# Performance work log

Hardware: AMD Instinct MI355X
Metric: run time of the kernel (lower is better)

## Reference

```python
import jax, jax.numpy as jnp
import numpy as np

L, B, D, V = 4096, 4, 512, 1000  # seq_len, batch, hidden_dim, index_dim


def setup_inputs() -> dict:
    key = jax.random.key(0)
    k0, k1, k2, k3, k4 = jax.random.split(key, 5)
    s_d = 1.0 / np.sqrt(D)
    return {
        "x": jax.random.normal(k0, (L, B, D), dtype=jnp.float32),
        # ctc_weight: nn.Linear(D, D)
        "Ww": jax.random.uniform(k1, (D, D), dtype=jnp.float32, minval=-s_d, maxval=s_d),
        "Wb": jax.random.uniform(k2, (D,), dtype=jnp.float32, minval=-s_d, maxval=s_d),
        # ctc_linear: nn.Linear(D, V)
        "Lw": jax.random.uniform(k3, (V, D), dtype=jnp.float32, minval=-s_d, maxval=s_d),
        "Lb": jax.random.uniform(k4, (V,), dtype=jnp.float32, minval=-s_d, maxval=s_d),
    }


def reference(x, Ww, Wb, Lw, Lb):
    # x: (L, B, D) -> (B, L, D)
    xb = jnp.transpose(x, (1, 0, 2))
    # ctc_weight(x): (B, L, D)
    wx = xb @ Ww.T + Wb
    # bmm(x, W(x)^T): (B, L, L) bilinear scores (no softmax)
    scores = jnp.einsum('bld,bmd->blm', xb, wx)
    # bmm(scores, x): (B, L, D)
    y = jnp.einsum('blm,bmd->bld', scores, xb)
    # ctc_linear + log_softmax over vocab
    logits = y @ Lw.T + Lb  # (B, L, V)
    out = jax.nn.log_softmax(logits, axis=2)
    # permute back to (L, B, V)
    return jnp.transpose(out, (1, 0, 2))
```

## Files before the change

kernel.cpp:

```cpp
#include <hip/hip_runtime.h>
#include <math.h>

#define L_ 4096
#define B_ 4
#define D_ 512
#define V_ 1000
#define VP 1024
#define BD 2048
#define NCH 8

typedef __attribute__((ext_vector_type(8))) short short8;
typedef __attribute__((ext_vector_type(4))) float f32x4;
typedef __attribute__((ext_vector_type(4))) short short4v;

__device__ __forceinline__ short f2bf(float f) {
  unsigned u = __float_as_uint(f);
  unsigned r = (u + 0x7FFFu + ((u >> 16) & 1u)) >> 16;
  return (short)r;
}
__device__ __forceinline__ float bf2f(short v) {
  return __uint_as_float(((unsigned)(unsigned short)v) << 16);
}

__global__ __launch_bounds__(256) void kPre(const float* __restrict__ x,
                                            const float* __restrict__ Wb,
                                            short* __restrict__ xbf,
                                            short* __restrict__ xT,
                                            float* __restrict__ s,
                                            float* __restrict__ c) {
  const int l0 = blockIdx.x * 64, d0 = blockIdx.y * 64, b = blockIdx.z;
  __shared__ short tile[64 * 72];
  const int tid = threadIdx.x;
  const int r = tid >> 2;
  const int q = tid & 3;
  const int c0 = q * 16;

  short sv[16];
  float cpart = 0.f;
  const float* src = x + (size_t)(l0 + r) * BD + b * D_ + d0 + c0;
#pragma unroll
  for (int qq = 0; qq < 4; ++qq) {
    float4 f = *(const float4*)(src + qq * 4);
    const float* wb = Wb + d0 + c0 + qq * 4;
    cpart += f.x * wb[0] + f.y * wb[1] + f.z * wb[2] + f.w * wb[3];
    sv[qq * 4 + 0] = f2bf(f.x); sv[qq * 4 + 1] = f2bf(f.y);
    sv[qq * 4 + 2] = f2bf(f.z); sv[qq * 4 + 3] = f2bf(f.w);
  }
  short* dst = xbf + ((size_t)b * L_ + l0 + r) * D_ + d0 + c0;
  *(short8*)(dst)     = *(short8*)(sv);
  *(short8*)(dst + 8) = *(short8*)(sv + 8);
#pragma unroll
  for (int i = 0; i < 16; ++i) tile[(c0 + i) * 72 + r] = sv[i];
  cpart += __shfl_xor(cpart, 1);
  cpart += __shfl_xor(cpart, 2);
  if (q == 0) atomicAdd(&c[b * L_ + l0 + r], cpart);
  __syncthreads();
  short8 t0 = *(const short8*)(tile + r * 72 + c0);
  short8 t1 = *(const short8*)(tile + r * 72 + c0 + 8);
  short* tdst = xT + ((size_t)b * D_ + d0 + r) * L_ + l0 + c0;
  *(short8*)(tdst)     = t0;
  *(short8*)(tdst + 8) = t1;
  float spart = 0.f;
#pragma unroll
  for (int i = 0; i < 8; ++i) spart += bf2f(t0[i]) + bf2f(t1[i]);
  spart += __shfl_xor(spart, 1);
  spart += __shfl_xor(spart, 2);
  if (q == 0) atomicAdd(&s[b * D_ + d0 + r], spart);
}

__global__ __launch_bounds__(256) void kCastW(const float* __restrict__ Ww,
                                              const float* __restrict__ Lw,
                                              short* __restrict__ Wwb,
                                              short* __restrict__ Lwb) {
  const int idx = blockIdx.x * 256 + threadIdx.x;
  if (idx < 65536) {
    const int e = idx * 4;
    float4 f = *(const float4*)(Ww + e);
    short4v o; o[0] = f2bf(f.x); o[1] = f2bf(f.y); o[2] = f2bf(f.z); o[3] = f2bf(f.w);
    *(short4v*)(Wwb + e) = o;
  } else {
    const int e = (idx - 65536) * 4;
    const int v = e >> 9;
    short4v o = {};
    if (v < V_) {
      float4 f = *(const float4*)(Lw + e);
      o[0] = f2bf(f.x); o[1] = f2bf(f.y); o[2] = f2bf(f.z); o[3] = f2bf(f.w);
    }
    *(short4v*)(Lwb + e) = o;
  }
}

__global__ __launch_bounds__(256) void kT(const float* __restrict__ Lw,
                                          const float* __restrict__ s,
                                          float* __restrict__ t) {
  const int w = threadIdx.x >> 6, lane = threadIdx.x & 63;
  const int wid = blockIdx.x * 4 + w;
  const int b = wid >> 10, v = wid & 1023;
  float sum = 0.f;
  if (v < V_) {
    const float* lr = Lw + (size_t)v * D_;
    const float* sb = s + b * D_;
#pragma unroll
    for (int i = 0; i < 8; ++i) sum += lr[lane + i * 64] * sb[lane + i * 64];
  }
  for (int off = 32; off; off >>= 1) sum += __shfl_down(sum, off);
  if (lane == 0) t[b * VP + v] = (v < V_) ? sum : 0.f;
}

__global__ __launch_bounds__(256) void kGbf(const short* __restrict__ xT,
                                            short* __restrict__ Gpart) {
  const int z = blockIdx.z;
  const int b = z >> 3, ch = z & 7;
  const int i0 = blockIdx.x * 128, j0 = blockIdx.y * 128;
  const short* Ab = xT + (size_t)b * D_ * L_;
  __shared__ short As[128 * 64];
  __shared__ short Bs[128 * 64];
  f32x4 acc[4][4] = {};
  const int tid = threadIdx.x;
  const int w = tid >> 6, lane = tid & 63;
  const int quad = lane >> 4, mcol = lane & 15;
  const int wr0 = (w & 1) * 64, wc0 = (w >> 1) * 64;
  const int kbase = ch * 512;

  for (int k0 = kbase; k0 < kbase + 512; k0 += 64) {
#pragma unroll
    for (int q = 0; q < 4; ++q) {
      const int u = q * 256 + tid;
      const int row = u >> 3, blk = u & 7;
      const int phys = blk ^ (row & 7);
      *(short8*)(As + row * 64 + phys * 8) =
          *(const short8*)(Ab + (size_t)(i0 + row) * L_ + k0 + blk * 8);
      *(short8*)(Bs + row * 64 + phys * 8) =
          *(const short8*)(Ab + (size_t)(j0 + row) * L_ + k0 + blk * 8);
    }
    __syncthreads();
#pragma unroll
    for (int ss = 0; ss < 2; ++ss) {
      short8 af[4], bf[4];
#pragma unroll
      for (int i = 0; i < 4; ++i) {
        const int arow = wr0 + i * 16 + mcol;
        const int ablk = (ss * 4 + quad) ^ (arow & 7);
        af[i] = *(const short8*)(As + arow * 64 + ablk * 8);
        const int brow = wc0 + i * 16 + mcol;
        const int bblk = (ss * 4 + quad) ^ (brow & 7);
        bf[i] = *(const short8*)(Bs + brow * 64 + bblk * 8);
      }
#pragma unroll
      for (int i = 0; i < 4; ++i)
#pragma unroll
        for (int j = 0; j < 4; ++j)
          acc[i][j] = __builtin_amdgcn_mfma_f32_16x16x32_bf16(af[i], bf[j],
                                                              acc[i][j], 0, 0, 0);
    }
    __syncthreads();
  }
  short* Gp = Gpart + (size_t)z * (D_ * D_);
#pragma unroll
  for (int i = 0; i < 4; ++i)
#pragma unroll
    for (int j = 0; j < 4; ++j) {
      const int col = j0 + wc0 + j * 16 + mcol;
#pragma unroll
      for (int r = 0; r < 4; ++r) {
        const int rowi = i0 + wr0 + i * 16 + quad * 4 + r;
        Gp[(size_t)rowi * D_ + col] = f2bf(acc[i][j][r]);
      }
    }
}

__global__ __launch_bounds__(256) void kGreduce(const short* __restrict__ Gpart,
                                                short* __restrict__ Gb) {
  const int idx = blockIdx.x * 256 + threadIdx.x;
  const int b = idx >> 15, e = (idx & 32767) * 8;
  float sum[8] = {};
#pragma unroll
  for (int ch = 0; ch < NCH; ++ch) {
    short8 v = *(const short8*)(Gpart + ((size_t)(b * NCH + ch)) * (D_ * D_) + e);
#pragma unroll
    for (int i = 0; i < 8; ++i) sum[i] += bf2f(v[i]);
  }
  short8 o;
#pragma unroll
  for (int i = 0; i < 8; ++i) o[i] = f2bf(sum[i]);
  *(short8*)(Gb + (size_t)b * (D_ * D_) + e) = o;
}

__global__ __launch_bounds__(256) void kMbf(const short* __restrict__ Wwb,
                                            const short* __restrict__ Gb,
                                            short* __restrict__ Mb) {
  const int b = blockIdx.z;
  const int i0 = blockIdx.x * 128, j0 = blockIdx.y * 128;
  const short* Bbase = Gb + (size_t)b * D_ * D_;
  __shared__ short As[128 * 64];
  __shared__ short Bs[128 * 64];
  f32x4 acc[4][4] = {};
  const int tid = threadIdx.x;
  const int w = tid >> 6, lane = tid & 63;
  const int quad = lane >> 4, mcol = lane & 15;
  const int wr0 = (w & 1) * 64, wc0 = (w >> 1) * 64;

  for (int k0 = 0; k0 < D_; k0 += 64) {
#pragma unroll
    for (int q = 0; q < 4; ++q) {
      const int u = q * 256 + tid;
      const int row = u >> 3, blk = u & 7;
      const int phys = blk ^ (row & 7);
      *(short8*)(As + row * 64 + phys * 8) =
          *(const short8*)(Wwb + (size_t)(i0 + row) * D_ + k0 + blk * 8);
      *(short8*)(Bs + row * 64 + phys * 8) =
          *(const short8*)(Bbase + (size_t)(j0 + row) * D_ + k0 + blk * 8);
    }
    __syncthreads();
#pragma unroll
    for (int ss = 0; ss < 2; ++ss) {
      short8 af[4], bf[4];
#pragma unroll
      for (int i = 0; i < 4; ++i) {
        const int arow = wr0 + i * 16 + mcol;
        const int ablk = (ss * 4 + quad) ^ (arow & 7);
        af[i] = *(const short8*)(As + arow * 64 + ablk * 8);
        const int brow = wc0 + i * 16 + mcol;
        const int bblk = (ss * 4 + quad) ^ (brow & 7);
        bf[i] = *(const short8*)(Bs + brow * 64 + bblk * 8);
      }
#pragma unroll
      for (int i = 0; i < 4; ++i)
#pragma unroll
        for (int j = 0; j < 4; ++j)
          acc[i][j] = __builtin_amdgcn_mfma_f32_16x16x32_bf16(af[i], bf[j],
                                                              acc[i][j], 0, 0, 0);
    }
    __syncthreads();
  }
  short* Mo = Mb + (size_t)b * D_ * D_;
#pragma unroll
  for (int i = 0; i < 4; ++i)
#pragma unroll
    for (int j = 0; j < 4; ++j) {
      const int col = j0 + wc0 + j * 16 + mcol;
#pragma unroll
      for (int r = 0; r < 4; ++r) {
        const int rowi = i0 + wr0 + i * 16 + quad * 4 + r;
        Mo[(size_t)rowi * D_ + col] = f2bf(acc[i][j][r]);
      }
    }
}

__global__ __launch_bounds__(256) void kPbf(const short* __restrict__ Lwb,
                                            const short* __restrict__ Mb,
                                            short* __restrict__ Ptb) {
  const int b = blockIdx.z;
  const int i0 = blockIdx.x * 128;
  const int j0 = blockIdx.y * 128;
  const short* Bbase = Mb + (size_t)b * D_ * D_;
  __shared__ short As[128 * 64];
  __shared__ short Bs[128 * 64];
  f32x4 acc[4][4] = {};
  const int tid = threadIdx.x;
  const int w = tid >> 6, lane = tid & 63;
  const int quad = lane >> 4, mcol = lane & 15;
  const int wr0 = (w & 1) * 64, wc0 = (w >> 1) * 64;

  for (int k0 = 0; k0 < D_; k0 += 64) {
#pragma unroll
    for (int q = 0; q < 4; ++q) {
      const int u = q * 256 + tid;
      const int row = u >> 3, blk = u & 7;
      const int phys = blk ^ (row & 7);
      *(short8*)(As + row * 64 + phys * 8) =
          *(const short8*)(Lwb + (size_t)(i0 + row) * D_ + k0 + blk * 8);
      *(short8*)(Bs + row * 64 + phys * 8) =
          *(const short8*)(Bbase + (size_t)(j0 + row) * D_ + k0 + blk * 8);
    }
    __syncthreads();
#pragma unroll
    for (int ss = 0; ss < 2; ++ss) {
      short8 af[4], bf[4];
#pragma unroll
      for (int i = 0; i < 4; ++i) {
        const int arow = wr0 + i * 16 + mcol;
        const int ablk = (ss * 4 + quad) ^ (arow & 7);
        af[i] = *(const short8*)(As + arow * 64 + ablk * 8);
        const int brow = wc0 + i * 16 + mcol;
        const int bblk = (ss * 4 + quad) ^ (brow & 7);
        bf[i] = *(const short8*)(Bs + brow * 64 + bblk * 8);
      }
#pragma unroll
      for (int i = 0; i < 4; ++i)
#pragma unroll
        for (int j = 0; j < 4; ++j)
          acc[i][j] = __builtin_amdgcn_mfma_f32_16x16x32_bf16(af[i], bf[j],
                                                              acc[i][j], 0, 0, 0);
    }
    __syncthreads();
  }
  short* Po = Ptb + (size_t)b * VP * D_;
#pragma unroll
  for (int i = 0; i < 4; ++i)
#pragma unroll
    for (int j = 0; j < 4; ++j) {
      const int col = j0 + wc0 + j * 16 + mcol;
#pragma unroll
      for (int r = 0; r < 4; ++r) {
        const int rowi = i0 + wr0 + i * 16 + quad * 4 + r;
        Po[(size_t)rowi * D_ + col] = f2bf(acc[i][j][r]);
      }
    }
}

__global__ __launch_bounds__(256) void kLogitsBf(const short* __restrict__ xbf,
                                                 const short* __restrict__ Ptb,
                                                 const float* __restrict__ c,
                                                 const float* __restrict__ t,
                                                 const float* __restrict__ Lb,
                                                 float* __restrict__ logits) {
  const int b = blockIdx.z;
  const int i0 = blockIdx.x * 128;
  const int j0 = blockIdx.y * 128;
  const short* Abase = xbf + (size_t)b * L_ * D_;
  const short* Bbase = Ptb + (size_t)b * VP * D_;
  __shared__ short As[128 * 64];
  __shared__ short Bs[128 * 64];
  f32x4 acc[4][4] = {};
  const int tid = threadIdx.x;
  const int w = tid >> 6, lane = tid & 63;
  const int quad = lane >> 4, mcol = lane & 15;
  const int wr0 = (w & 1) * 64, wc0 = (w >> 1) * 64;

  for (int k0 = 0; k0 < D_; k0 += 64) {
#pragma unroll
    for (int q = 0; q < 4; ++q) {
      const int u = q * 256 + tid;
      const int row = u >> 3, blk = u & 7;
      const int phys = blk ^ (row & 7);
      *(short8*)(As + row * 64 + phys * 8) =
          *(const short8*)(Abase + (size_t)(i0 + row) * D_ + k0 + blk * 8);
      *(short8*)(Bs + row * 64 + phys * 8) =
          *(const short8*)(Bbase + (size_t)(j0 + row) * D_ + k0 + blk * 8);
    }
    __syncthreads();
#pragma unroll
    for (int ss = 0; ss < 2; ++ss) {
      short8 af[4], bf[4];
#pragma unroll
      for (int i = 0; i < 4; ++i) {
        const int arow = wr0 + i * 16 + mcol;
        const int ablk = (ss * 4 + quad) ^ (arow & 7);
        af[i] = *(const short8*)(As + arow * 64 + ablk * 8);
        const int brow = wc0 + i * 16 + mcol;
        const int bblk = (ss * 4 + quad) ^ (brow & 7);
        bf[i] = *(const short8*)(Bs + brow * 64 + bblk * 8);
      }
#pragma unroll
      for (int i = 0; i < 4; ++i)
#pragma unroll
        for (int j = 0; j < 4; ++j)
          acc[i][j] = __builtin_amdgcn_mfma_f32_16x16x32_bf16(af[i], bf[j],
                                                              acc[i][j], 0, 0, 0);
    }
    __syncthreads();
  }
#pragma unroll
  for (int i = 0; i < 4; ++i)
#pragma unroll
    for (int j = 0; j < 4; ++j) {
      const int gv = j0 + wc0 + j * 16 + mcol;
      const float tv = t[b * VP + gv];
      const float lbv = (gv < V_) ? Lb[gv] : 0.f;
#pragma unroll
      for (int r = 0; r < 4; ++r) {
        const int gl = i0 + wr0 + i * 16 + quad * 4 + r;
        logits[((size_t)b * L_ + gl) * VP + gv] =
            acc[i][j][r] + c[b * L_ + gl] * tv + lbv;
      }
    }
}

__global__ __launch_bounds__(256) void kLsm(const float* __restrict__ logits,
                                            float* __restrict__ out) {
  const int l = blockIdx.x, b = blockIdx.y;
  const int tid = threadIdx.x;
  const int lane = tid & 63, w = tid >> 6;
  const float* row = logits + ((size_t)b * L_ + l) * VP;
  float vals[4];
  float vmax = -__builtin_inff();
#pragma unroll
  for (int j = 0; j < 4; ++j) {
    const int v = tid + j * 256;
    vals[j] = (v < V_) ? row[v] : -__builtin_inff();
    vmax = fmaxf(vmax, vals[j]);
  }
  for (int off = 32; off; off >>= 1) vmax = fmaxf(vmax, __shfl_down(vmax, off));
  __shared__ float red_max[4];
  __shared__ float red_sum[4];
  if (lane == 0) red_max[w] = vmax;
  __syncthreads();
  const float m = fmaxf(fmaxf(red_max[0], red_max[1]),
                        fmaxf(red_max[2], red_max[3]));
  float se = 0.f;
#pragma unroll
  for (int j = 0; j < 4; ++j) se += expf(vals[j] - m);
  for (int off = 32; off; off >>= 1) se += __shfl_down(se, off);
  if (lane == 0) red_sum[w] = se;
  __syncthreads();
  const float lse = m + logf(red_sum[0] + red_sum[1] + red_sum[2] + red_sum[3]);
  float* orow = out + (size_t)l * (B_ * V_) + b * V_;
#pragma unroll
  for (int j = 0; j < 4; ++j) {
    const int v = tid + j * 256;
    if (v < V_) orow[v] = vals[j] - lse;
  }
}

extern "C" void kernel_launch(void* const* d_in, const int* in_sizes, int n_in,
                              void* d_out, int out_size, void* d_ws,
                              size_t ws_size, hipStream_t stream) {
  const float* x  = (const float*)d_in[0];
  const float* Ww = (const float*)d_in[1];
  const float* Wb = (const float*)d_in[2];
  const float* Lw = (const float*)d_in[3];
  const float* Lb = (const float*)d_in[4];

  char* wp = (char*)d_ws;
  short* xbf = (short*)wp;   wp += (size_t)B_ * L_ * D_ * 2;
  short* xT  = (short*)wp;   wp += (size_t)B_ * L_ * D_ * 2;
  short* Ptb = (short*)wp;   wp += (size_t)B_ * VP * D_ * 2;
  short* Gpart = (short*)wp; wp += (size_t)B_ * NCH * D_ * D_ * 2;
  short* Gb  = (short*)wp;   wp += (size_t)B_ * D_ * D_ * 2;
  short* Mb  = (short*)wp;   wp += (size_t)B_ * D_ * D_ * 2;
  short* Wwb = (short*)wp;   wp += (size_t)D_ * D_ * 2;
  short* Lwb = (short*)wp;   wp += (size_t)VP * D_ * 2;
  float* s   = (float*)wp;   wp += (size_t)B_ * D_ * 4;
  float* c   = (float*)wp;   wp += (size_t)B_ * L_ * 4;
  float* t   = (float*)wp;   wp += (size_t)B_ * VP * 4;
  float* logits = (float*)wp;

  hipMemsetAsync(s, 0, (size_t)(B_ * D_ + B_ * L_) * sizeof(float), stream);

  kCastW<<<dim3(768), 256, 0, stream>>>(Ww, Lw, Wwb, Lwb);
  kPre<<<dim3(64, 8, B_), 256, 0, stream>>>(x, Wb, xbf, xT, s, c);
  kGbf<<<dim3(4, 4, B_ * NCH), 256, 0, stream>>>(xT, Gpart);
  kGreduce<<<dim3(512), 256, 0, stream>>>(Gpart, Gb);
  kMbf<<<dim3(4, 4, B_), 256, 0, stream>>>(Wwb, Gb, Mb);
  kT<<<dim3(1024), 256, 0, stream>>>(Lw, s, t);
  kPbf<<<dim3(8, 4, B_), 256, 0, stream>>>(Lwb, Mb, Ptb);
  kLogitsBf<<<dim3(32, 8, B_), 256, 0, stream>>>(xbf, Ptb, c, t, Lb, logits);
  kLsm<<<dim3(L_, B_), 256, 0, stream>>>(logits, (float*)d_out);
}
```

Before: 207.7 us.

## Fuse logits GEMM with log-softmax so logits never round-trip through memory

Replaces the separate logits GEMM and row-wise log-softmax kernels with one kernel. Each block computes a 32-row by full-vocab tile: it keeps the A rows in LDS and streams the B fragments straight from global memory. The softmax max and sum are then reduced across lanes and waves through shared memory before the output is written. This removes the 64MB fp32 logits write and read-back and one launch. In exchange, B is read without LDS staging, which may make the kernel bound by memory latency, and there are only 512 blocks.

```diff
diff --git a/kernel.cpp b/kernel.cpp
--- a/kernel.cpp
+++ b/kernel.cpp
@@ -7,6 +7,7 @@
 #define V_ 1000
 #define VP 1024
 #define BD 2048
+#define OUT_BV 4000
 #define NCH 8
 
 typedef __attribute__((ext_vector_type(8))) short short8;
@@ -309,108 +310,117 @@
     }
 }
 
-__global__ __launch_bounds__(256) void kLogitsBf(const short* __restrict__ xbf,
-                                                 const short* __restrict__ Ptb,
-                                                 const float* __restrict__ c,
-                                                 const float* __restrict__ t,
-                                                 const float* __restrict__ Lb,
-                                                 float* __restrict__ logits) {
-  const int b = blockIdx.z;
-  const int i0 = blockIdx.x * 128;
-  const int j0 = blockIdx.y * 128;
-  const short* Abase = xbf + (size_t)b * L_ * D_;
+__global__ __launch_bounds__(512) void kOut(const short* __restrict__ xbf,
+                                            const short* __restrict__ Ptb,
+                                            const float* __restrict__ c,
+                                            const float* __restrict__ t,
+                                            const float* __restrict__ Lb,
+                                            float* __restrict__ out) {
+  const int b = blockIdx.y;
+  const int l0 = blockIdx.x * 32;
+  const short* Abase = xbf + ((size_t)b * L_ + l0) * D_;
   const short* Bbase = Ptb + (size_t)b * VP * D_;
-  __shared__ short As[128 * 64];
-  __shared__ short Bs[128 * 64];
-  f32x4 acc[4][4] = {};
+  __shared__ short As[32 * 512];
+  __shared__ float red_m[32][8];
+  __shared__ float red_s[32][8];
   const int tid = threadIdx.x;
   const int w = tid >> 6, lane = tid & 63;
   const int quad = lane >> 4, mcol = lane & 15;
-  const int wr0 = (w & 1) * 64, wc0 = (w >> 1) * 64;
-
-  for (int k0 = 0; k0 < D_; k0 += 64) {
-#pragma unroll
-    for (int q = 0; q < 4; ++q) {
-      const int u = q * 256 + tid;
-      const int row = u >> 3, blk = u & 7;
-      const int phys = blk ^ (row & 7);
-      *(short8*)(As + row * 64 + phys * 8) =
-          *(const short8*)(Abase + (size_t)(i0 + row) * D_ + k0 + blk * 8);
-      *(short8*)(Bs + row * 64 + phys * 8) =
-          *(const short8*)(Bbase + (size_t)(j0 + row) * D_ + k0 + blk * 8);
-    }
-    __syncthreads();
-#pragma unroll
-    for (int ss = 0; ss < 2; ++ss) {
-      short8 af[4], bf[4];
-#pragma unroll
-      for (int i = 0; i < 4; ++i) {
-        const int arow = wr0 + i * 16 + mcol;
-        const int ablk = (ss * 4 + quad) ^ (arow & 7);
-        af[i] = *(const short8*)(As + arow * 64 + ablk * 8);
-        const int brow = wc0 + i * 16 + mcol;
-        const int bblk = (ss * 4 + quad) ^ (brow & 7);
-        bf[i] = *(const short8*)(Bs + brow * 64 + bblk * 8);
-      }
-#pragma unroll
-      for (int i = 0; i < 4; ++i)
-#pragma unroll
-        for (int j = 0; j < 4; ++j)
-          acc[i][j] = __builtin_amdgcn_mfma_f32_16x16x32_bf16(af[i], bf[j],
-                                                              acc[i][j], 0, 0, 0);
-    }
-    __syncthreads();
-  }
-#pragma unroll
-  for (int i = 0; i < 4; ++i)
-#pragma unroll
-    for (int j = 0; j < 4; ++j) {
-      const int gv = j0 + wc0 + j * 16 + mcol;
-      const float tv = t[b * VP + gv];
-      const float lbv = (gv < V_) ? Lb[gv] : 0.f;
-#pragma unroll
-      for (int r = 0; r < 4; ++r) {
-        const int gl = i0 + wr0 + i * 16 + quad * 4 + r;
-        logits[((size_t)b * L_ + gl) * VP + gv] =
-            acc[i][j][r] + c[b * L_ + gl] * tv + lbv;
-      }
-    }
-}
-
-__global__ __launch_bounds__(256) void kLsm(const float* __restrict__ logits,
-                                            float* __restrict__ out) {
-  const int l = blockIdx.x, b = blockIdx.y;
-  const int tid = threadIdx.x;
-  const int lane = tid & 63, w = tid >> 6;
-  const float* row = logits + ((size_t)b * L_ + l) * VP;
-  float vals[4];
-  float vmax = -__builtin_inff();
-#pragma unroll
-  for (int j = 0; j < 4; ++j) {
-    const int v = tid + j * 256;
-    vals[j] = (v < V_) ? row[v] : -__builtin_inff();
-    vmax = fmaxf(vmax, vals[j]);
-  }
-  for (int off = 32; off; off >>= 1) vmax = fmaxf(vmax, __shfl_down(vmax, off));
-  __shared__ float red_max[4];
-  __shared__ float red_sum[4];
-  if (lane == 0) red_max[w] = vmax;
+  const int v0 = w * 128;
+
+  for (int ci = tid; ci < 2048; ci += 512) {
+    const int row = ci >> 6, blk = ci & 63;
+    const int phys = blk ^ (row & 7);
+    *(short8*)(As + row * 512 + phys * 8) =
+        *(const short8*)(Abase + (size_t)row * D_ + blk * 8);
+  }
   __syncthreads();
-  const float m = fmaxf(fmaxf(red_max[0], red_max[1]),
-                        fmaxf(red_max[2], red_max[3]));
-  float se = 0.f;
-#pragma unroll
-  for (int j = 0; j < 4; ++j) se += expf(vals[j] - m);
-  for (int off = 32; off; off >>= 1) se += __shfl_down(se, off);
-  if (lane == 0) red_sum[w] = se;
+
+  f32x4 acc[2][8] = {};
+  for (int ks = 0; ks < 16; ++ks) {
+    const int k0 = ks * 32;
+    short8 bfr[8];
+#pragma unroll
+    for (int j = 0; j < 8; ++j)
+      bfr[j] = *(const short8*)(Bbase +
+                                (size_t)(v0 + j * 16 + mcol) * D_ + k0 + quad * 8);
+    short8 af[2];
+#pragma unroll
+    for (int i = 0; i < 2; ++i) {
+      const int arow = i * 16 + mcol;
+      const int ablk = (ks * 4 + quad) ^ (arow & 7);
+      af[i] = *(const short8*)(As + arow * 512 + ablk * 8);
+    }
+#pragma unroll
+    for (int i = 0; i < 2; ++i)
+#pragma unroll
+      for (int j = 0; j < 8; ++j)
+        acc[i][j] = __builtin_amdgcn_mfma_f32_16x16x32_bf16(af[i], bfr[j],
+                                                            acc[i][j], 0, 0, 0);
+  }
+
+  float cv[2][4];
+#pragma unroll
+  for (int i = 0; i < 2; ++i)
+#pragma unroll
+    for (int r = 0; r < 4; ++r)
+      cv[i][r] = c[b * L_ + l0 + i * 16 + quad * 4 + r];
+  float tv[8], lbv[8];
+  bool valid[8];
+#pragma unroll
+  for (int j = 0; j < 8; ++j) {
+    const int gv = v0 + j * 16 + mcol;
+    tv[j] = t[b * VP + gv];
+    valid[j] = gv < V_;
+    lbv[j] = valid[j] ? Lb[gv] : 0.f;
+  }
+#pragma unroll
+  for (int i = 0; i < 2; ++i)
+#pragma unroll
+    for (int j = 0; j < 8; ++j)
+#pragma unroll
+      for (int r = 0; r < 4; ++r)
+        acc[i][j][r] += cv[i][r] * tv[j] + lbv[j];
+
+#pragma unroll
+  for (int i = 0; i < 2; ++i)
+#pragma unroll
+    for (int r = 0; r < 4; ++r) {
+      float m = -__builtin_inff();
+#pragma unroll
+      for (int j = 0; j < 8; ++j)
+        if (valid[j]) m = fmaxf(m, acc[i][j][r]);
+      for (int off = 1; off <= 8; off <<= 1) m = fmaxf(m, __shfl_xor(m, off));
+      float sse = 0.f;
+#pragma unroll
+      for (int j = 0; j < 8; ++j)
+        if (valid[j]) sse += expf(acc[i][j][r] - m);
+      for (int off = 1; off <= 8; off <<= 1) sse += __shfl_xor(sse, off);
+      if (mcol == 0) {
+        const int row = i * 16 + quad * 4 + r;
+        red_m[row][w] = m;
+        red_s[row][w] = sse;
+      }
+    }
   __syncthreads();
-  const float lse = m + logf(red_sum[0] + red_sum[1] + red_sum[2] + red_sum[3]);
-  float* orow = out + (size_t)l * (B_ * V_) + b * V_;
-#pragma unroll
-  for (int j = 0; j < 4; ++j) {
-    const int v = tid + j * 256;
-    if (v < V_) orow[v] = vals[j] - lse;
-  }
+
+#pragma unroll
+  for (int i = 0; i < 2; ++i)
+#pragma unroll
+    for (int r = 0; r < 4; ++r) {
+      const int row = i * 16 + quad * 4 + r;
+      float M = -__builtin_inff();
+#pragma unroll
+      for (int ww = 0; ww < 8; ++ww) M = fmaxf(M, red_m[row][ww]);
+      float S = 0.f;
+#pragma unroll
+      for (int ww = 0; ww < 8; ++ww) S += red_s[row][ww] * expf(red_m[row][ww] - M);
+      const float lse = M + logf(S);
+      float* orow = out + (size_t)(l0 + row) * OUT_BV + b * V_;
+#pragma unroll
+      for (int j = 0; j < 8; ++j)
+        if (valid[j]) orow[v0 + j * 16 + mcol] = acc[i][j][r] - lse;
+    }
 }
 
 extern "C" void kernel_launch(void* const* d_in, const int* in_sizes, int n_in,
@@ -434,7 +444,6 @@
   float* s   = (float*)wp;   wp += (size_t)B_ * D_ * 4;
   float* c   = (float*)wp;   wp += (size_t)B_ * L_ * 4;
   float* t   = (float*)wp;   wp += (size_t)B_ * VP * 4;
-  float* logits = (float*)wp;
 
   hipMemsetAsync(s, 0, (size_t)(B_ * D_ + B_ * L_) * sizeof(float), stream);
 
@@ -445,6 +454,5 @@
   kMbf<<<dim3(4, 4, B_), 256, 0, stream>>>(Wwb, Gb, Mb);
   kT<<<dim3(1024), 256, 0, stream>>>(Lw, s, t);
   kPbf<<<dim3(8, 4, B_), 256, 0, stream>>>(Lwb, Mb, Ptb);
-  kLogitsBf<<<dim3(32, 8, B_), 256, 0, stream>>>(xbf, Ptb, c, t, Lb, logits);
-  kLsm<<<dim3(L_, B_), 256, 0, stream>>>(logits, (float*)d_out);
-}
+  kOut<<<dim3(L_ / 32, B_), 512, 0, stream>>>(xbf, Ptb, c, t, Lb, (float*)d_out);
+}
```

Result: slower. 237.6 us (+14.4%).

## Store intermediate logits as bf16 with vectorized stores and wave-per-row log-softmax

Applied to the files above, without the earlier changes.

The logits GEMM now swaps operand roles so that each lane holds four consecutive vocab entries, letting it write packed 4-element bf16 stores instead of scattered fp32 stores. The intermediate logits buffer is halved in size by storing bf16. The log-softmax kernel processes one row per wavefront with shuffle-xor reductions and no shared memory or block barriers, reading 16 bf16 values per lane and writing float4 outputs. Rounding the logits to bf16 before log-softmax adds precision loss in the output.

```diff
diff --git a/kernel.cpp b/kernel.cpp
--- a/kernel.cpp
+++ b/kernel.cpp
@@ -7,6 +7,7 @@
 #define V_ 1000
 #define VP 1024
 #define BD 2048
+#define OUT_BV 4000
 #define NCH 8
 
 typedef __attribute__((ext_vector_type(8))) short short8;
@@ -309,17 +310,17 @@
     }
 }
 
-__global__ __launch_bounds__(256) void kLogitsBf(const short* __restrict__ xbf,
-                                                 const short* __restrict__ Ptb,
-                                                 const float* __restrict__ c,
-                                                 const float* __restrict__ t,
-                                                 const float* __restrict__ Lb,
-                                                 float* __restrict__ logits) {
+__global__ __launch_bounds__(256) void kLogits2(const short* __restrict__ xbf,
+                                                const short* __restrict__ Ptb,
+                                                const float* __restrict__ c,
+                                                const float* __restrict__ t,
+                                                const float* __restrict__ Lb,
+                                                short* __restrict__ logitsBf) {
   const int b = blockIdx.z;
-  const int i0 = blockIdx.x * 128;
-  const int j0 = blockIdx.y * 128;
-  const short* Abase = xbf + (size_t)b * L_ * D_;
-  const short* Bbase = Ptb + (size_t)b * VP * D_;
+  const int v0t = blockIdx.x * 128;
+  const int l0t = blockIdx.y * 128;
+  const short* Abase = Ptb + (size_t)b * VP * D_;
+  const short* Bbase = xbf + (size_t)b * L_ * D_;
   __shared__ short As[128 * 64];
   __shared__ short Bs[128 * 64];
   f32x4 acc[4][4] = {};
@@ -335,9 +336,9 @@
       const int row = u >> 3, blk = u & 7;
       const int phys = blk ^ (row & 7);
       *(short8*)(As + row * 64 + phys * 8) =
-          *(const short8*)(Abase + (size_t)(i0 + row) * D_ + k0 + blk * 8);
+          *(const short8*)(Abase + (size_t)(v0t + row) * D_ + k0 + blk * 8);
       *(short8*)(Bs + row * 64 + phys * 8) =
-          *(const short8*)(Bbase + (size_t)(j0 + row) * D_ + k0 + blk * 8);
+          *(const short8*)(Bbase + (size_t)(l0t + row) * D_ + k0 + blk * 8);
     }
     __syncthreads();
 #pragma unroll
@@ -362,54 +363,55 @@
     __syncthreads();
   }
 #pragma unroll
-  for (int i = 0; i < 4; ++i)
-#pragma unroll
-    for (int j = 0; j < 4; ++j) {
-      const int gv = j0 + wc0 + j * 16 + mcol;
-      const float tv = t[b * VP + gv];
-      const float lbv = (gv < V_) ? Lb[gv] : 0.f;
-#pragma unroll
-      for (int r = 0; r < 4; ++r) {
-        const int gl = i0 + wr0 + i * 16 + quad * 4 + r;
-        logits[((size_t)b * L_ + gl) * VP + gv] =
-            acc[i][j][r] + c[b * L_ + gl] * tv + lbv;
-      }
-    }
-}
-
-__global__ __launch_bounds__(256) void kLsm(const float* __restrict__ logits,
+  for (int j = 0; j < 4; ++j) {
+    const int gl = l0t + wc0 + j * 16 + mcol;
+    const float cl = c[b * L_ + gl];
+#pragma unroll
+    for (int i = 0; i < 4; ++i) {
+      const int gv0 = v0t + wr0 + i * 16 + quad * 4;
+      f32x4 tv = *(const f32x4*)(t + b * VP + gv0);
+      f32x4 lb4 = {};
+      if (gv0 < V_) lb4 = *(const f32x4*)(Lb + gv0);
+      short4v o;
+#pragma unroll
+      for (int r = 0; r < 4; ++r)
+        o[r] = f2bf(acc[i][j][r] + cl * tv[r] + lb4[r]);
+      *(short4v*)(logitsBf + ((size_t)b * L_ + gl) * VP + gv0) = o;
+    }
+  }
+}
+
+__global__ __launch_bounds__(256) void kLsm(const short* __restrict__ logitsBf,
                                             float* __restrict__ out) {
-  const int l = blockIdx.x, b = blockIdx.y;
-  const int tid = threadIdx.x;
-  const int lane = tid & 63, w = tid >> 6;
-  const float* row = logits + ((size_t)b * L_ + l) * VP;
-  float vals[4];
-  float vmax = -__builtin_inff();
-#pragma unroll
-  for (int j = 0; j < 4; ++j) {
-    const int v = tid + j * 256;
-    vals[j] = (v < V_) ? row[v] : -__builtin_inff();
-    vmax = fmaxf(vmax, vals[j]);
-  }
-  for (int off = 32; off; off >>= 1) vmax = fmaxf(vmax, __shfl_down(vmax, off));
-  __shared__ float red_max[4];
-  __shared__ float red_sum[4];
-  if (lane == 0) red_max[w] = vmax;
-  __syncthreads();
-  const float m = fmaxf(fmaxf(red_max[0], red_max[1]),
-                        fmaxf(red_max[2], red_max[3]));
+  const int b = blockIdx.y;
+  const int l = blockIdx.x * 4 + (threadIdx.x >> 6);
+  const int lane = threadIdx.x & 63;
+  const short* row = logitsBf + ((size_t)b * L_ + l) * VP;
+  short8 v0 = *(const short8*)(row + lane * 16);
+  short8 v1 = *(const short8*)(row + lane * 16 + 8);
+  float vals[16];
+#pragma unroll
+  for (int i = 0; i < 8; ++i) { vals[i] = bf2f(v0[i]); vals[8 + i] = bf2f(v1[i]); }
+  float m = -__builtin_inff();
+#pragma unroll
+  for (int i = 0; i < 16; ++i)
+    if (lane * 16 + i < V_) m = fmaxf(m, vals[i]);
+  for (int off = 32; off; off >>= 1) m = fmaxf(m, __shfl_xor(m, off));
   float se = 0.f;
 #pragma unroll
-  for (int j = 0; j < 4; ++j) se += expf(vals[j] - m);
-  for (int off = 32; off; off >>= 1) se += __shfl_down(se, off);
-  if (lane == 0) red_sum[w] = se;
-  __syncthreads();
-  const float lse = m + logf(red_sum[0] + red_sum[1] + red_sum[2] + red_sum[3]);
-  float* orow = out + (size_t)l * (B_ * V_) + b * V_;
-#pragma unroll
-  for (int j = 0; j < 4; ++j) {
-    const int v = tid + j * 256;
-    if (v < V_) orow[v] = vals[j] - lse;
+  for (int i = 0; i < 16; ++i)
+    if (lane * 16 + i < V_) se += expf(vals[i] - m);
+  for (int off = 32; off; off >>= 1) se += __shfl_xor(se, off);
+  const float lse = m + logf(se);
+  float* orow = out + (size_t)l * OUT_BV + b * V_;
+#pragma unroll
+  for (int q = 0; q < 4; ++q) {
+    const int base = lane * 16 + q * 4;
+    if (base < V_) {
+      float4 st = make_float4(vals[q * 4 + 0] - lse, vals[q * 4 + 1] - lse,
+                              vals[q * 4 + 2] - lse, vals[q * 4 + 3] - lse);
+      *(float4*)(orow + base) = st;
+    }
   }
 }
 
@@ -434,7 +436,7 @@
   float* s   = (float*)wp;   wp += (size_t)B_ * D_ * 4;
   float* c   = (float*)wp;   wp += (size_t)B_ * L_ * 4;
   float* t   = (float*)wp;   wp += (size_t)B_ * VP * 4;
-  float* logits = (float*)wp;
+  short* logitsBf = (short*)wp;
 
   hipMemsetAsync(s, 0, (size_t)(B_ * D_ + B_ * L_) * sizeof(float), stream);
 
@@ -445,6 +447,6 @@
   kMbf<<<dim3(4, 4, B_), 256, 0, stream>>>(Wwb, Gb, Mb);
   kT<<<dim3(1024), 256, 0, stream>>>(Lw, s, t);
   kPbf<<<dim3(8, 4, B_), 256, 0, stream>>>(Lwb, Mb, Ptb);
-  kLogitsBf<<<dim3(32, 8, B_), 256, 0, stream>>>(xbf, Ptb, c, t, Lb, logits);
-  kLsm<<<dim3(L_, B_), 256, 0, stream>>>(logits, (float*)d_out);
-}
+  kLogits2<<<dim3(8, 32, B_), 256, 0, stream>>>(xbf, Ptb, c, t, Lb, logitsBf);
+  kLsm<<<dim3(L_ / 4, B_), 256, 0, stream>>>(logitsBf, (float*)d_out);
+}
```

After: 217.7 us. 1.05x slower.
